# Performance work log

Measured on AMD Instinct MI355X. Metric: run time of the kernel, lower is better.

## Reference

```python
import jax, jax.numpy as jnp
import numpy as np

B, S, D, H = 32, 512, 512, 512  # batch, seq_len, input_size, hidden_size


def setup_inputs() -> dict:
    key = jax.random.key(0)
    ks = jax.random.split(key, 16)
    k = 1.0 / np.sqrt(H)  # torch LSTMCell init range
    def u(kk, shape):
        return jax.random.uniform(kk, shape, jnp.float32, -k, k)
    inp = {"x": jax.random.normal(ks[0], (B, S, D), jnp.float32)}
    # layer 0 cells consume D; layer 1 cells consume 2H (bidirectional concat)
    specs = [("f0", D), ("b0", D), ("f1", 2 * H), ("b1", 2 * H)]
    i = 1
    for name, din in specs:
        inp[f"Wih_{name}"] = u(ks[i], (4 * H, din)); i += 1
        inp[f"Whh_{name}"] = u(ks[i], (4 * H, H)); i += 1
        inp[f"b_{name}"] = u(ks[i], (4 * H,)); i += 1  # b_ih + b_hh folded into one bias
    return inp


def _run_dir(x, Wih, Whh, b, reverse):
    """One direction of one layer. x: [B, S, Din] -> (outputs [B, S, H], h_N, c_N)."""
    bsz = x.shape[0]
    xs = jnp.swapaxes(x, 0, 1)               # [S, B, Din]
    gx = xs @ Wih.T + b                      # precompute input projections [S, B, 4H]

    def step(carry, g_in):
        h, c = carry
        g = g_in + h @ Whh.T                 # [B, 4H]
        i_g, f_g, g_g, o_g = jnp.split(g, 4, axis=-1)  # torch gate order i,f,g,o
        c = jax.nn.sigmoid(f_g) * c + jax.nn.sigmoid(i_g) * jnp.tanh(g_g)
        h = jax.nn.sigmoid(o_g) * jnp.tanh(c)
        return (h, c), h

    h0 = jnp.zeros((bsz, H), x.dtype)
    c0 = jnp.zeros_like(h0)
    (hN, cN), ys = jax.lax.scan(step, (h0, c0), gx, reverse=reverse)
    return jnp.swapaxes(ys, 0, 1), hN, cN    # ys returned in original time order


def reference(x, Wih_f0, Whh_f0, b_f0, Wih_b0, Whh_b0, b_b0,
              Wih_f1, Whh_f1, b_f1, Wih_b1, Whh_b1, b_b1):
    layers = [((Wih_f0, Whh_f0, b_f0), (Wih_b0, Whh_b0, b_b0)),
              ((Wih_f1, Whh_f1, b_f1), (Wih_b1, Whh_b1, b_b1))]
    out = x
    for pf, pb in layers:
        fwd_out, h_f, c_f = _run_dir(out, *pf, reverse=False)
        bwd_out, h_b, c_b = _run_dir(out, *pb, reverse=True)
        out = jnp.concatenate([fwd_out, bwd_out], axis=-1)  # [B, S, 2H]
    h_n = jnp.stack([h_f, h_b], axis=0)
    c_n = jnp.stack([c_f, c_b], axis=0)
    return out, (h_n, c_n)
```

## Files before the change

kernel.cpp:

```cpp
#include <hip/hip_runtime.h>
#include <cstdint>
#include <cstddef>

#define BB 32
#define SS 512
#define HH 512
#define NBD 64
#define JPB 8
#define WR 32
#define WST 520

typedef short v8s __attribute__((ext_vector_type(8)));
typedef float v4f __attribute__((ext_vector_type(4)));
typedef unsigned int v4u __attribute__((ext_vector_type(4)));
typedef unsigned long long u64t;

static __device__ __forceinline__ float b2f(unsigned short u) {
    union { unsigned int i; float f; } v; v.i = ((unsigned int)u) << 16; return v.f;
}
static __device__ __forceinline__ unsigned short f2b(float f) {
    union { float f; unsigned int i; } v; v.f = f;
    unsigned int u = v.i;
    return (unsigned short)((u + 0x7fffu + ((u >> 16) & 1u)) >> 16);
}
static __device__ __forceinline__ void split1(float f, short& hi, short& lo) {
    const unsigned short h = f2b(f);
    hi = (short)h;
    lo = (short)f2b(f - b2f(h));
}

#define MFMA(a, b, c) __builtin_amdgcn_mfma_f32_16x16x32_bf16((a), (b), (c), 0, 0, 0)

template<int DIN, bool L0>
__global__ __launch_bounds__(256, 1)
void lstm_layer(const void*  __restrict__ xin_,
                const float* __restrict__ Wih_f,
                const float* __restrict__ Whh_f,
                const float* __restrict__ b_f,
                const float* __restrict__ Wih_b,
                const float* __restrict__ Whh_b,
                const float* __restrict__ b_b,
                void*  __restrict__ yout_,
                u64t*  __restrict__ hrec,
                unsigned int* __restrict__ flags,
                float* __restrict__ hn,
                float* __restrict__ cn)
{
    constexpr int NKX = DIN / 32;
    constexpr int NKH = HH / 32;
    constexpr int XST = DIN + 8;

    extern __shared__ char smem[];
    unsigned short* WhhHi = (unsigned short*)smem;
    unsigned short* WihHi = WhhHi + WR * WST;
    unsigned short* hHi   = WihHi + WR * XST;

    const int tid   = threadIdx.x;
    const int dir   = blockIdx.x >> 6;
    const int jb    = blockIdx.x & 63;
    const int jbase = jb * JPB;

    const float* Wih = dir ? Wih_b : Wih_f;
    const float* Whh = dir ? Whh_b : Whh_f;
    const float* bv  = dir ? b_b  : b_f;

    {
        const int r = tid >> 3;
        const int R = (r & 3) * HH + jbase + (r >> 2);
        {
            const int c0 = (tid & 7) * 64;
            const float* src = Whh + (size_t)R * HH + c0;
            #pragma unroll
            for (int c = 0; c < 64; c += 8) {
                v8s hi;
                #pragma unroll
                for (int e = 0; e < 8; ++e) hi[e] = (short)f2b(src[c + e]);
                *(v8s*)(WhhHi + r * WST + c0 + c) = hi;
            }
        }
        {
            const int c0 = (tid & 7) * (DIN / 8);
            const float* src = Wih + (size_t)R * DIN + c0;
            #pragma unroll
            for (int c = 0; c < DIN / 8; c += 8) {
                v8s hi;
                #pragma unroll
                for (int e = 0; e < 8; ++e) hi[e] = (short)f2b(src[c + e]);
                *(v8s*)(WihHi + r * XST + c0 + c) = hi;
            }
        }
    }

    const int lane = tid & 63;
    const int wv   = tid >> 6;
    const int mi   = wv & 1;
    const int ni   = wv >> 1;
    const int g    = lane >> 4;
    const int rA   = lane & 15;

    const int brow = mi * 16 + rA;
    const int col  = ni * 16 + rA;
    const int jl   = col >> 2;
    const int p    = rA & 3;

    const float bi_ = bv[0 * HH + jbase + jl];
    const float bf_ = bv[1 * HH + jbase + jl];
    const float bg_ = bv[2 * HH + jbase + jl];
    const float bo_ = bv[3 * HH + jbase + jl];

    __syncthreads();

    const float*          aXf = L0 ? (const float*)xin_ + (size_t)brow * SS * DIN + 8 * g : nullptr;
    const unsigned short* aXb = L0 ? nullptr : (const unsigned short*)xin_ + (size_t)brow * SS * DIN + 8 * g;
    const unsigned short* bHh = WhhHi + col * WST + 8 * g;
    const unsigned short* bHx = WihHi + col * XST + 8 * g;

    unsigned int* fbase = flags + (size_t)dir * SS * 64;

    const int batch = mi * 16 + 4 * g + p;
    const int pq = tid & 63;
    const int r0 = tid >> 6;
    float creg = 0.f;

    for (int st = 0; st < SS; ++st) {
        const int t = dir ? (SS - 1 - st) : st;

        v4f acc0 = {0,0,0,0}, acc1 = {0,0,0,0};
        v4f acc4 = {0,0,0,0}, acc5 = {0,0,0,0};

        if (L0) {
            const float* aX = aXf + (size_t)t * DIN;
            #pragma unroll
            for (int kt = 0; kt < NKX; kt += 2) {
                v8s ah0, al0, ah1, al1;
                #pragma unroll
                for (int e = 0; e < 8; ++e) {
                    short h, l;
                    split1(aX[kt * 32 + e], h, l);       ah0[e] = h; al0[e] = l;
                    split1(aX[(kt + 1) * 32 + e], h, l); ah1[e] = h; al1[e] = l;
                }
                v8s wh0 = *(const v8s*)(bHx + kt * 32);
                v8s wh1 = *(const v8s*)(bHx + (kt + 1) * 32);
                acc0 = MFMA(ah0, wh0, acc0);
                acc1 = MFMA(ah1, wh1, acc1);
                acc4 = MFMA(al0, wh0, acc4);
                acc5 = MFMA(al1, wh1, acc5);
            }
        } else {
            const unsigned short* aX = aXb + (size_t)t * DIN;
            #pragma unroll
            for (int kt = 0; kt < NKX; kt += 2) {
                v8s a0 = *(const v8s*)(aX + kt * 32);
                v8s a1 = *(const v8s*)(aX + (kt + 1) * 32);
                v8s wh0 = *(const v8s*)(bHx + kt * 32);
                v8s wh1 = *(const v8s*)(bHx + (kt + 1) * 32);
                acc0 = MFMA(a0, wh0, acc0);
                acc1 = MFMA(a1, wh1, acc1);
            }
        }

        if (st > 0) {
            {
                const unsigned int* f = fbase + (size_t)(st - 1) * 64 + pq;
                int guard = 0;
                while (!__hip_atomic_load(f, __ATOMIC_RELAXED,
                                          __HIP_MEMORY_SCOPE_AGENT)) {
                    __builtin_amdgcn_s_sleep(1);
                    if (++guard > (1 << 26)) break;
                }
            }
            const char* hb = (const char*)(hrec
                + (size_t)(dir * 2 + ((st - 1) & 1)) * (BB * HH / 4))
                + (size_t)r0 * 1024 + (size_t)pq * 16;
            const char* p0 = hb;
            const char* p1 = hb + 1 * 4096;
            const char* p2 = hb + 2 * 4096;
            const char* p3 = hb + 3 * 4096;
            const char* p4 = hb + 4 * 4096;
            const char* p5 = hb + 5 * 4096;
            const char* p6 = hb + 6 * 4096;
            const char* p7 = hb + 7 * 4096;
            v4u v0, v1, v2, v3, v4, v5, v6, v7;
            asm volatile(
                "global_load_dwordx4 %[o0], %[a0], off sc1\n\t"
                "global_load_dwordx4 %[o1], %[a1], off sc1\n\t"
                "global_load_dwordx4 %[o2], %[a2], off sc1\n\t"
                "global_load_dwordx4 %[o3], %[a3], off sc1\n\t"
                "global_load_dwordx4 %[o4], %[a4], off sc1\n\t"
                "global_load_dwordx4 %[o5], %[a5], off sc1\n\t"
                "global_load_dwordx4 %[o6], %[a6], off sc1\n\t"
                "global_load_dwordx4 %[o7], %[a7], off sc1\n\t"
                "s_waitcnt vmcnt(0)"
                : [o0]"=&v"(v0), [o1]"=&v"(v1), [o2]"=&v"(v2), [o3]"=&v"(v3),
                  [o4]"=&v"(v4), [o5]"=&v"(v5), [o6]"=&v"(v6), [o7]"=&v"(v7)
                : [a0]"v"(p0), [a1]"v"(p1), [a2]"v"(p2), [a3]"v"(p3),
                  [a4]"v"(p4), [a5]"v"(p5), [a6]"v"(p6), [a7]"v"(p7)
                : "memory");
            __builtin_amdgcn_sched_barrier(0);

            unsigned short* dst = hHi + r0 * WST + 8 * pq;
            *(v4u*)(dst + 0 * 4 * WST) = v0;
            *(v4u*)(dst + 1 * 4 * WST) = v1;
            *(v4u*)(dst + 2 * 4 * WST) = v2;
            *(v4u*)(dst + 3 * 4 * WST) = v3;
            *(v4u*)(dst + 4 * 4 * WST) = v4;
            *(v4u*)(dst + 5 * 4 * WST) = v5;
            *(v4u*)(dst + 6 * 4 * WST) = v6;
            *(v4u*)(dst + 7 * 4 * WST) = v7;
            __syncthreads();

            const unsigned short* aHh = hHi + brow * WST + 8 * g;
            #pragma unroll
            for (int kt = 0; kt < NKH; kt += 2) {
                v8s ah0 = *(const v8s*)(aHh + kt * 32);
                v8s ah1 = *(const v8s*)(aHh + (kt + 1) * 32);
                v8s bh0 = *(const v8s*)(bHh + kt * 32);
                v8s bh1 = *(const v8s*)(bHh + (kt + 1) * 32);
                acc0 = MFMA(ah0, bh0, acc0);
                acc1 = MFMA(ah1, bh1, acc1);
            }
        }
        acc0 = acc0 + acc1;
        if (L0) acc0 += (acc4 + acc5);

        float pi_, pf_, pg_, po_;
        {
            const float x0 = acc0[0], x1 = acc0[1], x2 = acc0[2], x3 = acc0[3];
            const float n0 = __shfl_xor(x0, 1), n1 = __shfl_xor(x1, 1);
            const float n2 = __shfl_xor(x2, 1), n3 = __shfl_xor(x3, 1);
            const float a0 = (p & 1) ? n1 : x0;
            const float a1 = (p & 1) ? x1 : n0;
            const float a2 = (p & 1) ? n3 : x2;
            const float a3 = (p & 1) ? x3 : n2;
            const float m0 = __shfl_xor(a0, 2), m1 = __shfl_xor(a1, 2);
            const float m2 = __shfl_xor(a2, 2), m3 = __shfl_xor(a3, 2);
            pi_ = (p & 2) ? m2 : a0;
            pf_ = (p & 2) ? m3 : a1;
            pg_ = (p & 2) ? a2 : m0;
            po_ = (p & 2) ? a3 : m1;
        }

        {
            const float ig = 1.f / (1.f + __expf(-(pi_ + bi_)));
            const float fg = 1.f / (1.f + __expf(-(pf_ + bf_)));
            const float gg = tanhf(pg_ + bg_);
            const float og = 1.f / (1.f + __expf(-(po_ + bo_)));
            creg = fg * creg + ig * gg;
            const float h = og * tanhf(creg);
            const float hq1 = __shfl_xor(h, 4);
            const float hq2 = __shfl_xor(h, 8);
            const float hq3 = __shfl_xor(hq1, 8);

            if ((jl & 3) == 0) {
                const u64t pk = (u64t)f2b(h)
                              | ((u64t)f2b(hq1) << 16)
                              | ((u64t)f2b(hq2) << 32)
                              | ((u64t)f2b(hq3) << 48);
                u64t* hw = hrec + (size_t)(dir * 2 + (st & 1)) * (BB * HH / 4)
                         + (size_t)batch * (HH / 4) + ((jbase + jl) >> 2);
                __hip_atomic_store(hw, pk, __ATOMIC_RELAXED, __HIP_MEMORY_SCOPE_AGENT);
            }
            asm volatile("s_waitcnt vmcnt(0)" ::: "memory");
            __syncthreads();
            if (tid == 0)
                __hip_atomic_store(fbase + (size_t)st * 64 + jb, 1u,
                                   __ATOMIC_RELAXED, __HIP_MEMORY_SCOPE_AGENT);

            if (L0) {
                if ((jl & 1) == 0) {
                    const unsigned int pko = (unsigned int)f2b(h)
                                           | ((unsigned int)f2b(hq1) << 16);
                    *((unsigned int*)yout_ + (size_t)batch * SS * HH + (size_t)t * HH
                                           + dir * (HH / 2) + ((jbase + jl) >> 1)) = pko;
                }
            } else {
                ((float*)yout_)[((size_t)batch * SS + t) * (2 * HH) + dir * HH + jbase + jl] = h;
                if (st == SS - 1) {
                    hn[(dir * BB + batch) * HH + jbase + jl] = h;
                    cn[(dir * BB + batch) * HH + jbase + jl] = creg;
                }
            }
        }
    }
}

extern "C" void kernel_launch(void* const* d_in, const int* in_sizes, int n_in,
                              void* d_out, int out_size, void* d_ws, size_t ws_size,
                              hipStream_t stream) {
    (void)in_sizes; (void)n_in;

    const float* x      = (const float*)d_in[0];
    const float* Wih_f0 = (const float*)d_in[1];
    const float* Whh_f0 = (const float*)d_in[2];
    const float* b_f0   = (const float*)d_in[3];
    const float* Wih_b0 = (const float*)d_in[4];
    const float* Whh_b0 = (const float*)d_in[5];
    const float* b_b0   = (const float*)d_in[6];
    const float* Wih_f1 = (const float*)d_in[7];
    const float* Whh_f1 = (const float*)d_in[8];
    const float* b_f1   = (const float*)d_in[9];
    const float* Wih_b1 = (const float*)d_in[10];
    const float* Whh_b1 = (const float*)d_in[11];
    const float* b_b1   = (const float*)d_in[12];

    char* ws = (char*)d_ws;
    const size_t Y0B  = (size_t)BB * SS * 2 * HH * 2;
    const size_t FLG  = (size_t)2 * SS * 64 * 4;
    const size_t HREC = (size_t)2 * 2 * BB * (HH / 4) * 8;
    const size_t NEED = Y0B + 2 * FLG + HREC;
    if (ws_size < NEED) return;
    if ((size_t)out_size < (size_t)BB * SS * 2 * HH + 4 * BB * HH) return;

    unsigned short* y0     = (unsigned short*)(ws);
    unsigned int*   flags0 = (unsigned int*)(ws + Y0B);
    unsigned int*   flags1 = (unsigned int*)(ws + Y0B + FLG);
    u64t*           hrec   = (u64t*)(ws + Y0B + 2 * FLG);

    float* out = (float*)d_out;
    float* hn  = out + (size_t)BB * SS * 2 * HH;
    float* cn  = hn + 2 * BB * HH;

    hipMemsetAsync(ws + Y0B, 0, 2 * FLG, stream);

    constexpr int SMB0 = WR * WST * 2 + WR * (512 + 8) * 2 + BB * WST * 2;
    constexpr int SMB1 = WR * WST * 2 + WR * (1024 + 8) * 2 + BB * WST * 2;
    hipFuncSetAttribute(reinterpret_cast<const void*>(lstm_layer<512,  true>),
                        hipFuncAttributeMaxDynamicSharedMemorySize, SMB0);
    hipFuncSetAttribute(reinterpret_cast<const void*>(lstm_layer<1024, false>),
                        hipFuncAttributeMaxDynamicSharedMemorySize, SMB1);

    lstm_layer<512, true><<<128, 256, SMB0, stream>>>(
        x, Wih_f0, Whh_f0, b_f0, Wih_b0, Whh_b0, b_b0,
        (void*)y0, hrec, flags0, nullptr, nullptr);

    lstm_layer<1024, false><<<128, 256, SMB1, stream>>>(
        y0, Wih_f1, Whh_f1, b_f1, Wih_b1, Whh_b1, b_b1,
        (void*)out, hrec, flags1, hn, cn);
}
```

Before: 6.164 ms.

## Batch input projections for four timesteps per weight load in recurrent loop

```diff
diff --git a/kernel.cpp b/kernel.cpp
--- a/kernel.cpp
+++ b/kernel.cpp
@@ -122,162 +122,181 @@
     const int r0 = tid >> 6;
     float creg = 0.f;
 
-    for (int st = 0; st < SS; ++st) {
-        const int t = dir ? (SS - 1 - st) : st;
-
-        v4f acc0 = {0,0,0,0}, acc1 = {0,0,0,0};
-        v4f acc4 = {0,0,0,0}, acc5 = {0,0,0,0};
+    for (int st4 = 0; st4 < SS; st4 += 4) {
+
+        v4f gx0[4], gx1[4], gx4[4], gx5[4];
+        #pragma unroll
+        for (int ph = 0; ph < 4; ++ph) {
+            gx0[ph] = (v4f){0,0,0,0}; gx1[ph] = (v4f){0,0,0,0};
+            gx4[ph] = (v4f){0,0,0,0}; gx5[ph] = (v4f){0,0,0,0};
+        }
 
         if (L0) {
-            const float* aX = aXf + (size_t)t * DIN;
-            #pragma unroll
+            #pragma unroll 2
             for (int kt = 0; kt < NKX; kt += 2) {
-                v8s ah0, al0, ah1, al1;
-                #pragma unroll
-                for (int e = 0; e < 8; ++e) {
-                    short h, l;
-                    split1(aX[kt * 32 + e], h, l);       ah0[e] = h; al0[e] = l;
-                    split1(aX[(kt + 1) * 32 + e], h, l); ah1[e] = h; al1[e] = l;
-                }
                 v8s wh0 = *(const v8s*)(bHx + kt * 32);
                 v8s wh1 = *(const v8s*)(bHx + (kt + 1) * 32);
-                acc0 = MFMA(ah0, wh0, acc0);
-                acc1 = MFMA(ah1, wh1, acc1);
-                acc4 = MFMA(al0, wh0, acc4);
-                acc5 = MFMA(al1, wh1, acc5);
+                #pragma unroll
+                for (int ph = 0; ph < 4; ++ph) {
+                    const int t = dir ? (SS - 1 - (st4 + ph)) : (st4 + ph);
+                    const float* aX = aXf + (size_t)t * DIN;
+                    v8s ah0, al0, ah1, al1;
+                    #pragma unroll
+                    for (int e = 0; e < 8; ++e) {
+                        short h, l;
+                        split1(aX[kt * 32 + e], h, l);       ah0[e] = h; al0[e] = l;
+                        split1(aX[(kt + 1) * 32 + e], h, l); ah1[e] = h; al1[e] = l;
+                    }
+                    gx0[ph] = MFMA(ah0, wh0, gx0[ph]);
+                    gx1[ph] = MFMA(ah1, wh1, gx1[ph]);
+                    gx4[ph] = MFMA(al0, wh0, gx4[ph]);
+                    gx5[ph] = MFMA(al1, wh1, gx5[ph]);
+                }
             }
         } else {
-            const unsigned short* aX = aXb + (size_t)t * DIN;
-            #pragma unroll
+            #pragma unroll 2
             for (int kt = 0; kt < NKX; kt += 2) {
-                v8s a0 = *(const v8s*)(aX + kt * 32);
-                v8s a1 = *(const v8s*)(aX + (kt + 1) * 32);
                 v8s wh0 = *(const v8s*)(bHx + kt * 32);
                 v8s wh1 = *(const v8s*)(bHx + (kt + 1) * 32);
-                acc0 = MFMA(a0, wh0, acc0);
-                acc1 = MFMA(a1, wh1, acc1);
-            }
-        }
-
-        if (st > 0) {
+                #pragma unroll
+                for (int ph = 0; ph < 4; ++ph) {
+                    const int t = dir ? (SS - 1 - (st4 + ph)) : (st4 + ph);
+                    const unsigned short* aX = aXb + (size_t)t * DIN;
+                    v8s a0 = *(const v8s*)(aX + kt * 32);
+                    v8s a1 = *(const v8s*)(aX + (kt + 1) * 32);
+                    gx0[ph] = MFMA(a0, wh0, gx0[ph]);
+                    gx1[ph] = MFMA(a1, wh1, gx1[ph]);
+                }
+            }
+        }
+
+        #pragma unroll
+        for (int ph = 0; ph < 4; ++ph) {
+            const int st = st4 + ph;
+            const int t  = dir ? (SS - 1 - st) : st;
+
+            v4f acc0 = gx0[ph], acc1 = gx1[ph];
+
+            if (st > 0) {
+                {
+                    const unsigned int* f = fbase + (size_t)(st - 1) * 64 + pq;
+                    int guard = 0;
+                    while (!__hip_atomic_load(f, __ATOMIC_RELAXED,
+                                              __HIP_MEMORY_SCOPE_AGENT)) {
+                        __builtin_amdgcn_s_sleep(1);
+                        if (++guard > (1 << 26)) break;
+                    }
+                }
+                const char* hb = (const char*)(hrec
+                    + (size_t)(dir * 2 + ((st - 1) & 1)) * (BB * HH / 4))
+                    + (size_t)r0 * 1024 + (size_t)pq * 16;
+                const char* p0 = hb;
+                const char* p1 = hb + 1 * 4096;
+                const char* p2 = hb + 2 * 4096;
+                const char* p3 = hb + 3 * 4096;
+                const char* p4 = hb + 4 * 4096;
+                const char* p5 = hb + 5 * 4096;
+                const char* p6 = hb + 6 * 4096;
+                const char* p7 = hb + 7 * 4096;
+                v4u v0, v1, v2, v3, v4, v5, v6, v7;
+                asm volatile(
+                    "global_load_dwordx4 %[o0], %[a0], off sc1\n\t"
+                    "global_load_dwordx4 %[o1], %[a1], off sc1\n\t"
+                    "global_load_dwordx4 %[o2], %[a2], off sc1\n\t"
+                    "global_load_dwordx4 %[o3], %[a3], off sc1\n\t"
+                    "global_load_dwordx4 %[o4], %[a4], off sc1\n\t"
+                    "global_load_dwordx4 %[o5], %[a5], off sc1\n\t"
+                    "global_load_dwordx4 %[o6], %[a6], off sc1\n\t"
+                    "global_load_dwordx4 %[o7], %[a7], off sc1\n\t"
+                    "s_waitcnt vmcnt(0)"
+                    : [o0]"=&v"(v0), [o1]"=&v"(v1), [o2]"=&v"(v2), [o3]"=&v"(v3),
+                      [o4]"=&v"(v4), [o5]"=&v"(v5), [o6]"=&v"(v6), [o7]"=&v"(v7)
+                    : [a0]"v"(p0), [a1]"v"(p1), [a2]"v"(p2), [a3]"v"(p3),
+                      [a4]"v"(p4), [a5]"v"(p5), [a6]"v"(p6), [a7]"v"(p7)
+                    : "memory");
+                __builtin_amdgcn_sched_barrier(0);
+
+                unsigned short* dst = hHi + r0 * WST + 8 * pq;
+                *(v4u*)(dst + 0 * 4 * WST) = v0;
+                *(v4u*)(dst + 1 * 4 * WST) = v1;
+                *(v4u*)(dst + 2 * 4 * WST) = v2;
+                *(v4u*)(dst + 3 * 4 * WST) = v3;
+                *(v4u*)(dst + 4 * 4 * WST) = v4;
+                *(v4u*)(dst + 5 * 4 * WST) = v5;
+                *(v4u*)(dst + 6 * 4 * WST) = v6;
+                *(v4u*)(dst + 7 * 4 * WST) = v7;
+                __syncthreads();
+
+                const unsigned short* aHh = hHi + brow * WST + 8 * g;
+                #pragma unroll
+                for (int kt = 0; kt < NKH; kt += 2) {
+                    v8s ah0 = *(const v8s*)(aHh + kt * 32);
+                    v8s ah1 = *(const v8s*)(aHh + (kt + 1) * 32);
+                    v8s bh0 = *(const v8s*)(bHh + kt * 32);
+                    v8s bh1 = *(const v8s*)(bHh + (kt + 1) * 32);
+                    acc0 = MFMA(ah0, bh0, acc0);
+                    acc1 = MFMA(ah1, bh1, acc1);
+                }
+            }
+            acc0 = acc0 + acc1;
+            if (L0) acc0 += (gx4[ph] + gx5[ph]);
+
+            float pi_, pf_, pg_, po_;
             {
-                const unsigned int* f = fbase + (size_t)(st - 1) * 64 + pq;
-                int guard = 0;
-                while (!__hip_atomic_load(f, __ATOMIC_RELAXED,
-                                          __HIP_MEMORY_SCOPE_AGENT)) {
-                    __builtin_amdgcn_s_sleep(1);
-                    if (++guard > (1 << 26)) break;
-                }
-            }
-            const char* hb = (const char*)(hrec
-                + (size_t)(dir * 2 + ((st - 1) & 1)) * (BB * HH / 4))
-                + (size_t)r0 * 1024 + (size_t)pq * 16;
-            const char* p0 = hb;
-            const char* p1 = hb + 1 * 4096;
-            const char* p2 = hb + 2 * 4096;
-            const char* p3 = hb + 3 * 4096;
-            const char* p4 = hb + 4 * 4096;
-            const char* p5 = hb + 5 * 4096;
-            const char* p6 = hb + 6 * 4096;
-            const char* p7 = hb + 7 * 4096;
-            v4u v0, v1, v2, v3, v4, v5, v6, v7;
-            asm volatile(
-                "global_load_dwordx4 %[o0], %[a0], off sc1\n\t"
-                "global_load_dwordx4 %[o1], %[a1], off sc1\n\t"
-                "global_load_dwordx4 %[o2], %[a2], off sc1\n\t"
-                "global_load_dwordx4 %[o3], %[a3], off sc1\n\t"
-                "global_load_dwordx4 %[o4], %[a4], off sc1\n\t"
-                "global_load_dwordx4 %[o5], %[a5], off sc1\n\t"
-                "global_load_dwordx4 %[o6], %[a6], off sc1\n\t"
-                "global_load_dwordx4 %[o7], %[a7], off sc1\n\t"
-                "s_waitcnt vmcnt(0)"
-                : [o0]"=&v"(v0), [o1]"=&v"(v1), [o2]"=&v"(v2), [o3]"=&v"(v3),
-                  [o4]"=&v"(v4), [o5]"=&v"(v5), [o6]"=&v"(v6), [o7]"=&v"(v7)
-                : [a0]"v"(p0), [a1]"v"(p1), [a2]"v"(p2), [a3]"v"(p3),
-                  [a4]"v"(p4), [a5]"v"(p5), [a6]"v"(p6), [a7]"v"(p7)
-                : "memory");
-            __builtin_amdgcn_sched_barrier(0);
-
-            unsigned short* dst = hHi + r0 * WST + 8 * pq;
-            *(v4u*)(dst + 0 * 4 * WST) = v0;
-            *(v4u*)(dst + 1 * 4 * WST) = v1;
-            *(v4u*)(dst + 2 * 4 * WST) = v2;
-            *(v4u*)(dst + 3 * 4 * WST) = v3;
-            *(v4u*)(dst + 4 * 4 * WST) = v4;
-            *(v4u*)(dst + 5 * 4 * WST) = v5;
-            *(v4u*)(dst + 6 * 4 * WST) = v6;
-            *(v4u*)(dst + 7 * 4 * WST) = v7;
-            __syncthreads();
-
-            const unsigned short* aHh = hHi + brow * WST + 8 * g;
-            #pragma unroll
-            for (int kt = 0; kt < NKH; kt += 2) {
-                v8s ah0 = *(const v8s*)(aHh + kt * 32);
-                v8s ah1 = *(const v8s*)(aHh + (kt + 1) * 32);
-                v8s bh0 = *(const v8s*)(bHh + kt * 32);
-                v8s bh1 = *(const v8s*)(bHh + (kt + 1) * 32);
-                acc0 = MFMA(ah0, bh0, acc0);
-                acc1 = MFMA(ah1, bh1, acc1);
-            }
-        }
-        acc0 = acc0 + acc1;
-        if (L0) acc0 += (acc4 + acc5);
-
-        float pi_, pf_, pg_, po_;
-        {
-            const float x0 = acc0[0], x1 = acc0[1], x2 = acc0[2], x3 = acc0[3];
-            const float n0 = __shfl_xor(x0, 1), n1 = __shfl_xor(x1, 1);
-            const float n2 = __shfl_xor(x2, 1), n3 = __shfl_xor(x3, 1);
-            const float a0 = (p & 1) ? n1 : x0;
-            const float a1 = (p & 1) ? x1 : n0;
-            const float a2 = (p & 1) ? n3 : x2;
-            const float a3 = (p & 1) ? x3 : n2;
-            const float m0 = __shfl_xor(a0, 2), m1 = __shfl_xor(a1, 2);
-            const float m2 = __shfl_xor(a2, 2), m3 = __shfl_xor(a3, 2);
-            pi_ = (p & 2) ? m2 : a0;
-            pf_ = (p & 2) ? m3 : a1;
-            pg_ = (p & 2) ? a2 : m0;
-            po_ = (p & 2) ? a3 : m1;
-        }
-
-        {
-            const float ig = 1.f / (1.f + __expf(-(pi_ + bi_)));
-            const float fg = 1.f / (1.f + __expf(-(pf_ + bf_)));
-            const float gg = tanhf(pg_ + bg_);
-            const float og = 1.f / (1.f + __expf(-(po_ + bo_)));
-            creg = fg * creg + ig * gg;
-            const float h = og * tanhf(creg);
-            const float hq1 = __shfl_xor(h, 4);
-            const float hq2 = __shfl_xor(h, 8);
-            const float hq3 = __shfl_xor(hq1, 8);
-
-            if ((jl & 3) == 0) {
-                const u64t pk = (u64t)f2b(h)
-                              | ((u64t)f2b(hq1) << 16)
-                              | ((u64t)f2b(hq2) << 32)
-                              | ((u64t)f2b(hq3) << 48);
-                u64t* hw = hrec + (size_t)(dir * 2 + (st & 1)) * (BB * HH / 4)
-                         + (size_t)batch * (HH / 4) + ((jbase + jl) >> 2);
-                __hip_atomic_store(hw, pk, __ATOMIC_RELAXED, __HIP_MEMORY_SCOPE_AGENT);
-            }
-            asm volatile("s_waitcnt vmcnt(0)" ::: "memory");
-            __syncthreads();
-            if (tid == 0)
-                __hip_atomic_store(fbase + (size_t)st * 64 + jb, 1u,
-                                   __ATOMIC_RELAXED, __HIP_MEMORY_SCOPE_AGENT);
-
-            if (L0) {
-                if ((jl & 1) == 0) {
-                    const unsigned int pko = (unsigned int)f2b(h)
-                                           | ((unsigned int)f2b(hq1) << 16);
-                    *((unsigned int*)yout_ + (size_t)batch * SS * HH + (size_t)t * HH
-                                           + dir * (HH / 2) + ((jbase + jl) >> 1)) = pko;
-                }
-            } else {
-                ((float*)yout_)[((size_t)batch * SS + t) * (2 * HH) + dir * HH + jbase + jl] = h;
-                if (st == SS - 1) {
-                    hn[(dir * BB + batch) * HH + jbase + jl] = h;
-                    cn[(dir * BB + batch) * HH + jbase + jl] = creg;
+                const float x0 = acc0[0], x1 = acc0[1], x2 = acc0[2], x3 = acc0[3];
+                const float n0 = __shfl_xor(x0, 1), n1 = __shfl_xor(x1, 1);
+                const float n2 = __shfl_xor(x2, 1), n3 = __shfl_xor(x3, 1);
+                const float a0 = (p & 1) ? n1 : x0;
+                const float a1 = (p & 1) ? x1 : n0;
+                const float a2 = (p & 1) ? n3 : x2;
+                const float a3 = (p & 1) ? x3 : n2;
+                const float m0 = __shfl_xor(a0, 2), m1 = __shfl_xor(a1, 2);
+                const float m2 = __shfl_xor(a2, 2), m3 = __shfl_xor(a3, 2);
+                pi_ = (p & 2) ? m2 : a0;
+                pf_ = (p & 2) ? m3 : a1;
+                pg_ = (p & 2) ? a2 : m0;
+                po_ = (p & 2) ? a3 : m1;
+            }
+
+            {
+                const float ig = 1.f / (1.f + __expf(-(pi_ + bi_)));
+                const float fg = 1.f / (1.f + __expf(-(pf_ + bf_)));
+                const float gg = tanhf(pg_ + bg_);
+                const float og = 1.f / (1.f + __expf(-(po_ + bo_)));
+                creg = fg * creg + ig * gg;
+                const float h = og * tanhf(creg);
+                const float hq1 = __shfl_xor(h, 4);
+                const float hq2 = __shfl_xor(h, 8);
+                const float hq3 = __shfl_xor(hq1, 8);
+
+                if ((jl & 3) == 0) {
+                    const u64t pk = (u64t)f2b(h)
+                                  | ((u64t)f2b(hq1) << 16)
+                                  | ((u64t)f2b(hq2) << 32)
+                                  | ((u64t)f2b(hq3) << 48);
+                    u64t* hw = hrec + (size_t)(dir * 2 + (st & 1)) * (BB * HH / 4)
+                             + (size_t)batch * (HH / 4) + ((jbase + jl) >> 2);
+                    __hip_atomic_store(hw, pk, __ATOMIC_RELAXED, __HIP_MEMORY_SCOPE_AGENT);
+                }
+                asm volatile("s_waitcnt vmcnt(0)" ::: "memory");
+                __syncthreads();
+                if (tid == 0)
+                    __hip_atomic_store(fbase + (size_t)st * 64 + jb, 1u,
+                                       __ATOMIC_RELAXED, __HIP_MEMORY_SCOPE_AGENT);
+
+                if (L0) {
+                    if ((jl & 1) == 0) {
+                        const unsigned int pko = (unsigned int)f2b(h)
+                                               | ((unsigned int)f2b(hq1) << 16);
+                        *((unsigned int*)yout_ + (size_t)batch * SS * HH + (size_t)t * HH
+                                               + dir * (HH / 2) + ((jbase + jl) >> 1)) = pko;
+                    }
+                } else {
+                    ((float*)yout_)[((size_t)batch * SS + t) * (2 * HH) + dir * HH + jbase + jl] = h;
+                    if (st == SS - 1) {
+                        hn[(dir * BB + batch) * HH + jbase + jl] = h;
+                        cn[(dir * BB + batch) * HH + jbase + jl] = creg;
+                    }
                 }
             }
         }
```

New measurement: 9.787 ms. +58.8%, slower.

## Split persistent LSTM blocks by batch halves with wider hidden slices

Applied to the files above, without the earlier changes.

```diff
diff --git a/kernel.cpp b/kernel.cpp
--- a/kernel.cpp
+++ b/kernel.cpp
@@ -5,9 +5,8 @@
 #define BB 32
 #define SS 512
 #define HH 512
-#define NBD 64
-#define JPB 8
-#define WR 32
+#define JPB 16
+#define WR 64
 #define WST 520
 
 typedef short v8s __attribute__((ext_vector_type(8)));
@@ -30,6 +29,24 @@
 }
 
 #define MFMA(a, b, c) __builtin_amdgcn_mfma_f32_16x16x32_bf16((a), (b), (c), 0, 0, 0)
+
+__global__ void wih1_presplit(const float* __restrict__ Wf,
+                              const float* __restrict__ Wb,
+                              unsigned short* __restrict__ whi)
+{
+    const size_t n = (size_t)2 * 2048 * 512;
+    for (size_t i = (size_t)blockIdx.x * blockDim.x + threadIdx.x; i < n;
+         i += (size_t)gridDim.x * blockDim.x) {
+        const int dir = (int)(i >> 20);
+        const size_t rem = i & ((1u << 20) - 1);
+        const int rp = (int)(rem >> 9);
+        const int kk = (int)(rem & 511);
+        const int jb = rp >> 6;
+        const int r  = rp & 63;
+        const int R  = (r & 3) * HH + jb * JPB + (r >> 2);
+        whi[i] = f2b((dir ? Wb : Wf)[(size_t)R * 1024 + 512 + kk]);
+    }
+}
 
 template<int DIN, bool L0>
 __global__ __launch_bounds__(256, 1)
@@ -40,6 +57,7 @@
                 const float* __restrict__ Wih_b,
                 const float* __restrict__ Whh_b,
                 const float* __restrict__ b_b,
+                const unsigned short* __restrict__ wsp,
                 void*  __restrict__ yout_,
                 u64t*  __restrict__ hrec,
                 unsigned int* __restrict__ flags,
@@ -47,17 +65,16 @@
                 float* __restrict__ cn)
 {
     constexpr int NKX = DIN / 32;
-    constexpr int NKH = HH / 32;
-    constexpr int XST = DIN + 8;
 
     extern __shared__ char smem[];
     unsigned short* WhhHi = (unsigned short*)smem;
     unsigned short* WihHi = WhhHi + WR * WST;
-    unsigned short* hHi   = WihHi + WR * XST;
+    unsigned short* hHi   = WihHi + WR * WST;
 
     const int tid   = threadIdx.x;
     const int dir   = blockIdx.x >> 6;
-    const int jb    = blockIdx.x & 63;
+    const int grp   = (blockIdx.x >> 5) & 1;
+    const int jb    = blockIdx.x & 31;
     const int jbase = jb * JPB;
 
     const float* Wih = dir ? Wih_b : Wih_f;
@@ -65,13 +82,13 @@
     const float* bv  = dir ? b_b  : b_f;
 
     {
-        const int r = tid >> 3;
-        const int R = (r & 3) * HH + jbase + (r >> 2);
+        const int r  = tid >> 2;
+        const int c0 = (tid & 3) * 128;
+        const int R  = (r & 3) * HH + jbase + (r >> 2);
         {
-            const int c0 = (tid & 7) * 64;
             const float* src = Whh + (size_t)R * HH + c0;
             #pragma unroll
-            for (int c = 0; c < 64; c += 8) {
+            for (int c = 0; c < 128; c += 8) {
                 v8s hi;
                 #pragma unroll
                 for (int e = 0; e < 8; ++e) hi[e] = (short)f2b(src[c + e]);
@@ -79,27 +96,23 @@
             }
         }
         {
-            const int c0 = (tid & 7) * (DIN / 8);
             const float* src = Wih + (size_t)R * DIN + c0;
             #pragma unroll
-            for (int c = 0; c < DIN / 8; c += 8) {
+            for (int c = 0; c < 128; c += 8) {
                 v8s hi;
                 #pragma unroll
                 for (int e = 0; e < 8; ++e) hi[e] = (short)f2b(src[c + e]);
-                *(v8s*)(WihHi + r * XST + c0 + c) = hi;
+                *(v8s*)(WihHi + r * WST + c0 + c) = hi;
             }
         }
     }
 
     const int lane = tid & 63;
     const int wv   = tid >> 6;
-    const int mi   = wv & 1;
-    const int ni   = wv >> 1;
     const int g    = lane >> 4;
     const int rA   = lane & 15;
 
-    const int brow = mi * 16 + rA;
-    const int col  = ni * 16 + rA;
+    const int col  = wv * 16 + rA;
     const int jl   = col >> 2;
     const int p    = rA & 3;
 
@@ -110,16 +123,22 @@
 
     __syncthreads();
 
-    const float*          aXf = L0 ? (const float*)xin_ + (size_t)brow * SS * DIN + 8 * g : nullptr;
-    const unsigned short* aXb = L0 ? nullptr : (const unsigned short*)xin_ + (size_t)brow * SS * DIN + 8 * g;
+    const int abatch = grp * 16 + rA;
+    const float*          aXf = L0 ? (const float*)xin_ + (size_t)abatch * SS * DIN + 8 * g : nullptr;
+    const unsigned short* aXb = L0 ? nullptr : (const unsigned short*)xin_ + (size_t)abatch * SS * DIN + 8 * g;
     const unsigned short* bHh = WhhHi + col * WST + 8 * g;
-    const unsigned short* bHx = WihHi + col * XST + 8 * g;
-
-    unsigned int* fbase = flags + (size_t)dir * SS * 64;
-
-    const int batch = mi * 16 + 4 * g + p;
-    const int pq = tid & 63;
-    const int r0 = tid >> 6;
+    const unsigned short* bHx = WihHi + col * WST + 8 * g;
+    const unsigned short* wspL = L0 ? nullptr
+        : wsp + ((size_t)(dir * 2048 + jb * 64 + col)) * 512 + 8 * g;
+
+    unsigned int* fbase = flags + (size_t)(dir * 2 + grp) * SS * 64;
+    u64t* hrbase = hrec + (size_t)(dir * 2 + grp) * 2 * (16 * 128);
+
+    const int batch  = 4 * g + p;
+    const int gbatch = grp * 16 + batch;
+    const int c16 = tid & 63;
+    const int r0s = tid >> 6;
+    const int prod = c16 >> 1;
     float creg = 0.f;
 
     for (int st = 0; st < SS; ++st) {
@@ -149,7 +168,7 @@
         } else {
             const unsigned short* aX = aXb + (size_t)t * DIN;
             #pragma unroll
-            for (int kt = 0; kt < NKX; kt += 2) {
+            for (int kt = 0; kt < 16; kt += 2) {
                 v8s a0 = *(const v8s*)(aX + kt * 32);
                 v8s a1 = *(const v8s*)(aX + (kt + 1) * 32);
                 v8s wh0 = *(const v8s*)(bHx + kt * 32);
@@ -157,11 +176,20 @@
                 acc0 = MFMA(a0, wh0, acc0);
                 acc1 = MFMA(a1, wh1, acc1);
             }
+            #pragma unroll
+            for (int kt = 16; kt < 32; kt += 2) {
+                v8s a0 = *(const v8s*)(aX + kt * 32);
+                v8s a1 = *(const v8s*)(aX + (kt + 1) * 32);
+                v8s wh0 = *(const v8s*)(wspL + (kt - 16) * 32);
+                v8s wh1 = *(const v8s*)(wspL + (kt - 15) * 32);
+                acc0 = MFMA(a0, wh0, acc0);
+                acc1 = MFMA(a1, wh1, acc1);
+            }
         }
 
         if (st > 0) {
             {
-                const unsigned int* f = fbase + (size_t)(st - 1) * 64 + pq;
+                const unsigned int* f = fbase + (size_t)(st - 1) * 64 + prod;
                 int guard = 0;
                 while (!__hip_atomic_load(f, __ATOMIC_RELAXED,
                                           __HIP_MEMORY_SCOPE_AGENT)) {
@@ -169,49 +197,34 @@
                     if (++guard > (1 << 26)) break;
                 }
             }
-            const char* hb = (const char*)(hrec
-                + (size_t)(dir * 2 + ((st - 1) & 1)) * (BB * HH / 4))
-                + (size_t)r0 * 1024 + (size_t)pq * 16;
+            const char* hb = (const char*)(hrbase + ((st - 1) & 1) * (16 * 128))
+                           + (size_t)r0s * 1024 + (size_t)c16 * 16;
             const char* p0 = hb;
             const char* p1 = hb + 1 * 4096;
             const char* p2 = hb + 2 * 4096;
             const char* p3 = hb + 3 * 4096;
-            const char* p4 = hb + 4 * 4096;
-            const char* p5 = hb + 5 * 4096;
-            const char* p6 = hb + 6 * 4096;
-            const char* p7 = hb + 7 * 4096;
-            v4u v0, v1, v2, v3, v4, v5, v6, v7;
+            v4u v0, v1, v2, v3;
             asm volatile(
                 "global_load_dwordx4 %[o0], %[a0], off sc1\n\t"
                 "global_load_dwordx4 %[o1], %[a1], off sc1\n\t"
                 "global_load_dwordx4 %[o2], %[a2], off sc1\n\t"
                 "global_load_dwordx4 %[o3], %[a3], off sc1\n\t"
-                "global_load_dwordx4 %[o4], %[a4], off sc1\n\t"
-                "global_load_dwordx4 %[o5], %[a5], off sc1\n\t"
-                "global_load_dwordx4 %[o6], %[a6], off sc1\n\t"
-                "global_load_dwordx4 %[o7], %[a7], off sc1\n\t"
                 "s_waitcnt vmcnt(0)"
-                : [o0]"=&v"(v0), [o1]"=&v"(v1), [o2]"=&v"(v2), [o3]"=&v"(v3),
-                  [o4]"=&v"(v4), [o5]"=&v"(v5), [o6]"=&v"(v6), [o7]"=&v"(v7)
-                : [a0]"v"(p0), [a1]"v"(p1), [a2]"v"(p2), [a3]"v"(p3),
-                  [a4]"v"(p4), [a5]"v"(p5), [a6]"v"(p6), [a7]"v"(p7)
+                : [o0]"=&v"(v0), [o1]"=&v"(v1), [o2]"=&v"(v2), [o3]"=&v"(v3)
+                : [a0]"v"(p0), [a1]"v"(p1), [a2]"v"(p2), [a3]"v"(p3)
                 : "memory");
             __builtin_amdgcn_sched_barrier(0);
 
-            unsigned short* dst = hHi + r0 * WST + 8 * pq;
+            unsigned short* dst = hHi + r0s * WST + 8 * c16;
             *(v4u*)(dst + 0 * 4 * WST) = v0;
             *(v4u*)(dst + 1 * 4 * WST) = v1;
             *(v4u*)(dst + 2 * 4 * WST) = v2;
             *(v4u*)(dst + 3 * 4 * WST) = v3;
-            *(v4u*)(dst + 4 * 4 * WST) = v4;
-            *(v4u*)(dst + 5 * 4 * WST) = v5;
-            *(v4u*)(dst + 6 * 4 * WST) = v6;
-            *(v4u*)(dst + 7 * 4 * WST) = v7;
             __syncthreads();
 
-            const unsigned short* aHh = hHi + brow * WST + 8 * g;
-            #pragma unroll
-            for (int kt = 0; kt < NKH; kt += 2) {
+            const unsigned short* aHh = hHi + rA * WST + 8 * g;
+            #pragma unroll
+            for (int kt = 0; kt < 16; kt += 2) {
                 v8s ah0 = *(const v8s*)(aHh + kt * 32);
                 v8s ah1 = *(const v8s*)(aHh + (kt + 1) * 32);
                 v8s bh0 = *(const v8s*)(bHh + kt * 32);
@@ -256,8 +269,8 @@
                               | ((u64t)f2b(hq1) << 16)
                               | ((u64t)f2b(hq2) << 32)
                               | ((u64t)f2b(hq3) << 48);
-                u64t* hw = hrec + (size_t)(dir * 2 + (st & 1)) * (BB * HH / 4)
-                         + (size_t)batch * (HH / 4) + ((jbase + jl) >> 2);
+                u64t* hw = hrbase + (st & 1) * (16 * 128)
+                         + (size_t)batch * 128 + ((jbase + jl) >> 2);
                 __hip_atomic_store(hw, pk, __ATOMIC_RELAXED, __HIP_MEMORY_SCOPE_AGENT);
             }
             asm volatile("s_waitcnt vmcnt(0)" ::: "memory");
@@ -270,14 +283,14 @@
                 if ((jl & 1) == 0) {
                     const unsigned int pko = (unsigned int)f2b(h)
                                            | ((unsigned int)f2b(hq1) << 16);
-                    *((unsigned int*)yout_ + (size_t)batch * SS * HH + (size_t)t * HH
+                    *((unsigned int*)yout_ + (size_t)gbatch * SS * HH + (size_t)t * HH
                                            + dir * (HH / 2) + ((jbase + jl) >> 1)) = pko;
                 }
             } else {
-                ((float*)yout_)[((size_t)batch * SS + t) * (2 * HH) + dir * HH + jbase + jl] = h;
+                ((float*)yout_)[((size_t)gbatch * SS + t) * (2 * HH) + dir * HH + jbase + jl] = h;
                 if (st == SS - 1) {
-                    hn[(dir * BB + batch) * HH + jbase + jl] = h;
-                    cn[(dir * BB + batch) * HH + jbase + jl] = creg;
+                    hn[(dir * BB + gbatch) * HH + jbase + jl] = h;
+                    cn[(dir * BB + gbatch) * HH + jbase + jl] = creg;
                 }
             }
         }
@@ -305,9 +318,10 @@
 
     char* ws = (char*)d_ws;
     const size_t Y0B  = (size_t)BB * SS * 2 * HH * 2;
-    const size_t FLG  = (size_t)2 * SS * 64 * 4;
-    const size_t HREC = (size_t)2 * 2 * BB * (HH / 4) * 8;
-    const size_t NEED = Y0B + 2 * FLG + HREC;
+    const size_t FLG  = (size_t)2 * 2 * SS * 64 * 4;
+    const size_t HREC = (size_t)2 * 2 * 2 * 16 * 128 * 8;
+    const size_t WSP  = (size_t)2 * 2048 * 512 * 2;
+    const size_t NEED = Y0B + 2 * FLG + HREC + WSP;
     if (ws_size < NEED) return;
     if ((size_t)out_size < (size_t)BB * SS * 2 * HH + 4 * BB * HH) return;
 
@@ -315,6 +329,7 @@
     unsigned int*   flags0 = (unsigned int*)(ws + Y0B);
     unsigned int*   flags1 = (unsigned int*)(ws + Y0B + FLG);
     u64t*           hrec   = (u64t*)(ws + Y0B + 2 * FLG);
+    unsigned short* wsp    = (unsigned short*)(ws + Y0B + 2 * FLG + HREC);
 
     float* out = (float*)d_out;
     float* hn  = out + (size_t)BB * SS * 2 * HH;
@@ -322,18 +337,19 @@
 
     hipMemsetAsync(ws + Y0B, 0, 2 * FLG, stream);
 
-    constexpr int SMB0 = WR * WST * 2 + WR * (512 + 8) * 2 + BB * WST * 2;
-    constexpr int SMB1 = WR * WST * 2 + WR * (1024 + 8) * 2 + BB * WST * 2;
+    wih1_presplit<<<1024, 256, 0, stream>>>(Wih_f1, Wih_b1, wsp);
+
+    constexpr int SMB = WR * WST * 2 + WR * WST * 2 + 16 * WST * 2;
     hipFuncSetAttribute(reinterpret_cast<const void*>(lstm_layer<512,  true>),
-                        hipFuncAttributeMaxDynamicSharedMemorySize, SMB0);
+                        hipFuncAttributeMaxDynamicSharedMemorySize, SMB);
     hipFuncSetAttribute(reinterpret_cast<const void*>(lstm_layer<1024, false>),
-                        hipFuncAttributeMaxDynamicSharedMemorySize, SMB1);
-
-    lstm_layer<512, true><<<128, 256, SMB0, stream>>>(
+                        hipFuncAttributeMaxDynamicSharedMemorySize, SMB);
+
+    lstm_layer<512, true><<<128, 256, SMB, stream>>>(
         x, Wih_f0, Whh_f0, b_f0, Wih_b0, Whh_b0, b_b0,
-        (void*)y0, hrec, flags0, nullptr, nullptr);
-
-    lstm_layer<1024, false><<<128, 256, SMB1, stream>>>(
+        nullptr, (void*)y0, hrec, flags0, nullptr, nullptr);
+
+    lstm_layer<1024, false><<<128, 256, SMB, stream>>>(
         y0, Wih_f1, Whh_f1, b_f1, Wih_b1, Whh_b1, b_b1,
-        (void*)out, hrec, flags1, hn, cn);
-}
+        wsp, (void*)out, hrec, flags1, hn, cn);
+}
```

Measured after the change: 6.796 ms. 1.1x slower.
